# Kernel tuning notes

Measured on AMD Instinct MI355X. Metric: run time of the kernel, lower is better.

The kernel has to match this reference:

```python
import jax, jax.numpy as jnp
import numpy as np

PI = 3.1415926
CHAINS = [[0, 2, 5, 8, 11], [0, 1, 4, 7, 10], [0, 3, 6, 9, 12, 15], [9, 14, 17, 19, 21], [9, 13, 16, 18, 20]]
NUM_JOINTS = 22
CTX = 512
B = 131072


def setup_inputs() -> dict:
    key = jax.random.key(0)
    k_ctx, k_w0, k_b0, k_w, k_b = jax.random.split(key, 5)
    context_vec = jax.random.normal(k_ctx, (B, CTX), dtype=jnp.float32)
    # root linear: context_size -> 3
    W0 = jax.random.normal(k_w0, (CTX, 3), dtype=jnp.float32) * 0.02
    b0 = jax.random.normal(k_b0, (3,), dtype=jnp.float32) * 0.02
    # non-root linears: (context_size + 3) -> 3, stacked per joint index (row 0 unused)
    W = jax.random.normal(k_w, (NUM_JOINTS, CTX + 3, 3), dtype=jnp.float32) * 0.02
    b = jax.random.normal(k_b, (NUM_JOINTS, 3), dtype=jnp.float32) * 0.02
    return {"context_vec": context_vec, "W0": W0, "b0": b0, "W": W, "b": b}


def reference(context_vec, W0, b0, W, b):
    # Sequential per-joint tiny linears along kinematic chains (do_all_parent=False):
    # each child consumes [context, parent_joint(3)] -> 3, then tanh * PI.
    joints = [None] * NUM_JOINTS
    joints[0] = jnp.tanh(context_vec @ W0 + b0) * PI  # [B, 3]
    for chain in CHAINS:
        for j in range(1, len(chain)):
            jid = chain[j]
            inp = jnp.concatenate([context_vec, joints[chain[j - 1]]], axis=-1)  # [B, CTX+3]
            joints[jid] = jnp.tanh(inp @ W[jid] + b[jid]) * PI
    return jnp.concatenate(joints, axis=-1)  # [B, 3*NUM_JOINTS]
```

## Files before the change

### kernel.cpp

```cpp
#include <hip/hip_runtime.h>
#include <cstdint>
#include <cstddef>


#define CTXD 512
#define NCOL 66
#define KT   16
#define NT   5
#define NCH  8
#define RPB  128
#define LDS_STRIDE 67

typedef __attribute__((ext_vector_type(8))) short  short8;
typedef __attribute__((ext_vector_type(4))) float  f32x4;

__device__ __forceinline__ unsigned short f2bf(float x) {
  unsigned u = __float_as_uint(x);
  return (unsigned short)((u + 0x7FFFu + ((u >> 16) & 1u)) >> 16);
}

__device__ __forceinline__ unsigned cvt2(float a, float b) {
  unsigned r;
  asm("v_cvt_pk_bf16_f32 %0, %1, %2" : "=v"(r) : "v"(a), "v"(b));
  return r;
}

__device__ __forceinline__ float tanhpi(float x) {
  float t = exp2f(x * 2.885390081777927f);
  return 3.1415926f - 6.2831852f * __builtin_amdgcn_rcpf(t + 1.0f);
}

__global__ void prep_wfrag(const float* __restrict__ W0,
                           const float* __restrict__ W,
                           unsigned short* __restrict__ wf) {
  int idx = blockIdx.x * blockDim.x + threadIdx.x;
  if (idx >= KT * NT * 64 * 8) return;
  int j    = idx & 7;
  int lane = (idx >> 3) & 63;
  int rest = idx >> 9;
  int nt   = rest % NT;
  int kt   = rest / NT;
  int k    = kt * 32 + (lane >> 4) * 8 + j;
  int col  = nt * 16 + (lane & 15);
  float v = 0.f;
  if (col < 3)          v = W0[k * 3 + col];
  else if (col < NCOL)  v = W[(col / 3) * (515 * 3) + k * 3 + (col % 3)];
  wf[idx] = f2bf(v);
}

__global__ __launch_bounds__(256, 4) void hdl_main(
    const float* __restrict__ ctx,
    const float* __restrict__ b0,
    const float* __restrict__ W,
    const float* __restrict__ bflat,
    const unsigned short* __restrict__ wf,
    float* __restrict__ out)
{
  __shared__ float smem[RPB * LDS_STRIDE];

  const int tid  = threadIdx.x;
  const int lane = tid & 63;
  const int wave = tid >> 6;
  const int r16  = lane & 15;
  const int kg   = lane >> 4;
  const long blockRow = (long)blockIdx.x * RPB;

  f32x4 acc[2][NT] = {};

  float bias[NT];
#pragma unroll
  for (int n = 0; n < NT; ++n) {
    int col = n * 16 + r16;
    bias[n] = (col < 3) ? b0[col] : ((col < NCOL) ? bflat[col] : 0.f);
  }

  float* stage = smem + wave * 2048;
  const float* srcBase =
      ctx + (blockRow + wave * 32 + (lane >> 4)) * (long)CTXD + (lane & 15) * 4;

  for (int c = 0; c < NCH; ++c) {
#pragma unroll
    for (int j = 0; j < 8; ++j) {
      const float* s = srcBase + (size_t)j * 4 * CTXD + c * 64;
      __builtin_amdgcn_global_load_lds(
          (const __attribute__((address_space(1))) void*)s,
          (__attribute__((address_space(3))) void*)(stage + j * 256),
          16, 0, 0);
    }
    asm volatile("s_waitcnt vmcnt(0)" ::: "memory");

#pragma unroll
    for (int t = 0; t < 2; ++t) {
      const int kt = c * 2 + t;
      short8 bfr[NT];
#pragma unroll
      for (int n = 0; n < NT; ++n)
        bfr[n] = *(const short8*)(wf + (size_t)((kt * NT + n) * 64 + lane) * 8);

#pragma unroll
      for (int m = 0; m < 2; ++m) {
        const float* fp = stage + (m * 16 + r16) * 64 + t * 32 + kg * 8;
        float4 f0 = *(const float4*)(fp);
        float4 f1 = *(const float4*)(fp + 4);
        union { short8 s; unsigned u[4]; } A;
        A.u[0] = cvt2(f0.x, f0.y);
        A.u[1] = cvt2(f0.z, f0.w);
        A.u[2] = cvt2(f1.x, f1.y);
        A.u[3] = cvt2(f1.z, f1.w);
#pragma unroll
        for (int n = 0; n < NT; ++n)
          acc[m][n] = __builtin_amdgcn_mfma_f32_16x16x32_bf16(
              A.s, bfr[n], acc[m][n], 0, 0, 0);
      }
    }
    asm volatile("" ::: "memory");
  }

  __syncthreads();

#pragma unroll
  for (int m = 0; m < 2; ++m) {
#pragma unroll
    for (int n = 0; n < NT; ++n) {
      int col = n * 16 + r16;
      if (col < NCOL) {
        int rb = wave * 32 + m * 16 + kg * 4;
#pragma unroll
        for (int q = 0; q < 4; ++q)
          smem[(rb + q) * LDS_STRIDE + col] = acc[m][n][q] + bias[n];
      }
    }
  }
  __syncthreads();

  if (tid < RPB) {
    float* row = smem + tid * LDS_STRIDE;
    float J[22][3];
#pragma unroll
    for (int cc = 0; cc < 3; ++cc) J[0][cc] = tanhpi(row[cc]);

    constexpr int EP[21] = {0,2,5,8, 0,1,4,7, 0,3,6,9,12, 9,14,17,19, 9,13,16,18};
    constexpr int EC[21] = {2,5,8,11, 1,4,7,10, 3,6,9,12,15, 14,17,19,21, 13,16,18,20};
#pragma unroll
    for (int e = 0; e < 21; ++e) {
      const int p  = EP[e];
      const int ch = EC[e];
      const float* wp = W + ch * 1545 + 1536;
#pragma unroll
      for (int cc = 0; cc < 3; ++cc) {
        float s = row[3 * ch + cc];
        s += J[p][0] * wp[cc] + J[p][1] * wp[3 + cc] + J[p][2] * wp[6 + cc];
        J[ch][cc] = tanhpi(s);
      }
    }
#pragma unroll
    for (int jj = 0; jj < 22; ++jj)
#pragma unroll
      for (int cc = 0; cc < 3; ++cc) row[3 * jj + cc] = J[jj][cc];
  }
  __syncthreads();

  const size_t outBase = (size_t)blockRow * NCOL;
  for (int i = tid; i < RPB * NCOL; i += 256) {
    int r = i / NCOL;
    int cc = i - r * NCOL;
    out[outBase + i] = smem[r * LDS_STRIDE + cc];
  }
}

extern "C" void kernel_launch(void* const* d_in, const int* in_sizes, int n_in,
                              void* d_out, int out_size, void* d_ws, size_t ws_size,
                              hipStream_t stream) {
  const float* ctx  = (const float*)d_in[0];
  const float* W0   = (const float*)d_in[1];
  const float* b0   = (const float*)d_in[2];
  const float* W    = (const float*)d_in[3];
  const float* bfl  = (const float*)d_in[4];
  unsigned short* wf = (unsigned short*)d_ws;

  int prep_elems = KT * NT * 64 * 8;
  hipLaunchKernelGGL(prep_wfrag, dim3((prep_elems + 255) / 256), dim3(256), 0,
                     stream, W0, W, wf);

  int nrows = out_size / NCOL;
  hipLaunchKernelGGL(hdl_main, dim3(nrows / RPB), dim3(256), 0,
                     stream, ctx, b0, W, bfl, wf, (float*)d_out);
}
```

Baseline: 64.04 us.

## Double-buffer per-wave LDS staging with XOR-swizzled layout

Result: no change. 63.73 us (-0.5%).

```diff
diff --git a/kernel.cpp b/kernel.cpp
--- a/kernel.cpp
+++ b/kernel.cpp
@@ -7,7 +7,6 @@
 #define NCOL 66
 #define KT   16
 #define NT   5
-#define NCH  8
 #define RPB  128
 #define LDS_STRIDE 67
 
@@ -76,44 +75,57 @@
 
   float* stage = smem + wave * 2048;
   const float* srcBase =
-      ctx + (blockRow + wave * 32 + (lane >> 4)) * (long)CTXD + (lane & 15) * 4;
-
-  for (int c = 0; c < NCH; ++c) {
-#pragma unroll
-    for (int j = 0; j < 8; ++j) {
-      const float* s = srcBase + (size_t)j * 4 * CTXD + c * 64;
-      __builtin_amdgcn_global_load_lds(
-          (const __attribute__((address_space(1))) void*)s,
-          (__attribute__((address_space(3))) void*)(stage + j * 256),
-          16, 0, 0);
-    }
-    asm volatile("s_waitcnt vmcnt(0)" ::: "memory");
-
-#pragma unroll
-    for (int t = 0; t < 2; ++t) {
-      const int kt = c * 2 + t;
-      short8 bfr[NT];
+      ctx + (blockRow + wave * 32 + (lane >> 3)) * (long)CTXD
+          + (((lane & 7) ^ (lane >> 3)) << 2);
+
+#define ISSUE_GLL(ktv, buf)                                                    \
+  {                                                                            \
+    _Pragma("unroll")                                                          \
+    for (int j = 0; j < 4; ++j) {                                              \
+      const float* s = srcBase + (size_t)(j * 8) * CTXD + (ktv) * 32;          \
+      __builtin_amdgcn_global_load_lds(                                        \
+          (const __attribute__((address_space(1))) void*)s,                    \
+          (__attribute__((address_space(3))) void*)((buf) + j * 256),          \
+          16, 0, 0);                                                           \
+    }                                                                          \
+  }
+
+  ISSUE_GLL(0, stage)
+
+#pragma unroll
+  for (int kt = 0; kt < KT; ++kt) {
+    const float* cur = stage + (kt & 1) * 1024;
+    float* nxt = stage + ((kt + 1) & 1) * 1024;
+
+    short8 bfr[NT];
+#pragma unroll
+    for (int n = 0; n < NT; ++n)
+      bfr[n] = *(const short8*)(wf + (size_t)((kt * NT + n) * 64 + lane) * 8);
+
+    if (kt < KT - 1) {
+      ISSUE_GLL(kt + 1, nxt)
+      asm volatile("s_waitcnt vmcnt(4)" ::: "memory");
+    } else {
+      asm volatile("s_waitcnt vmcnt(0)" ::: "memory");
+    }
+
+#pragma unroll
+    for (int m = 0; m < 2; ++m) {
+      const int row = m * 16 + r16;
+      const float* rbase = cur + row * 32;
+      const int rx = r16 & 7;
+      float4 f0 = *(const float4*)(rbase + ((((kg * 2)     ) ^ rx) << 2));
+      float4 f1 = *(const float4*)(rbase + ((((kg * 2) + 1 ) ^ rx) << 2));
+      union { short8 s; unsigned u[4]; } A;
+      A.u[0] = cvt2(f0.x, f0.y);
+      A.u[1] = cvt2(f0.z, f0.w);
+      A.u[2] = cvt2(f1.x, f1.y);
+      A.u[3] = cvt2(f1.z, f1.w);
 #pragma unroll
       for (int n = 0; n < NT; ++n)
-        bfr[n] = *(const short8*)(wf + (size_t)((kt * NT + n) * 64 + lane) * 8);
-
-#pragma unroll
-      for (int m = 0; m < 2; ++m) {
-        const float* fp = stage + (m * 16 + r16) * 64 + t * 32 + kg * 8;
-        float4 f0 = *(const float4*)(fp);
-        float4 f1 = *(const float4*)(fp + 4);
-        union { short8 s; unsigned u[4]; } A;
-        A.u[0] = cvt2(f0.x, f0.y);
-        A.u[1] = cvt2(f0.z, f0.w);
-        A.u[2] = cvt2(f1.x, f1.y);
-        A.u[3] = cvt2(f1.z, f1.w);
-#pragma unroll
-        for (int n = 0; n < NT; ++n)
-          acc[m][n] = __builtin_amdgcn_mfma_f32_16x16x32_bf16(
-              A.s, bfr[n], acc[m][n], 0, 0, 0);
-      }
-    }
-    asm volatile("" ::: "memory");
+        acc[m][n] = __builtin_amdgcn_mfma_f32_16x16x32_bf16(
+            A.s, bfr[n], acc[m][n], 0, 0, 0);
+    }
   }
 
   __syncthreads();
```

## Switch to single-wave blocks of 16 rows with full-row async LDS staging

Applied to the files above, without the earlier changes.

Measured after the change: 112.4 us. 1.76x slower.

```diff
diff --git a/kernel.cpp b/kernel.cpp
--- a/kernel.cpp
+++ b/kernel.cpp
@@ -7,8 +7,7 @@
 #define NCOL 66
 #define KT   16
 #define NT   5
-#define NCH  8
-#define RPB  128
+#define RPB  16
 #define LDS_STRIDE 67
 
 typedef __attribute__((ext_vector_type(8))) short  short8;
@@ -48,7 +47,7 @@
   wf[idx] = f2bf(v);
 }
 
-__global__ __launch_bounds__(256, 4) void hdl_main(
+__global__ __launch_bounds__(64) void hdl_main(
     const float* __restrict__ ctx,
     const float* __restrict__ b0,
     const float* __restrict__ W,
@@ -56,16 +55,68 @@
     const unsigned short* __restrict__ wf,
     float* __restrict__ out)
 {
-  __shared__ float smem[RPB * LDS_STRIDE];
+  __shared__ float smem[RPB * CTXD];
 
-  const int tid  = threadIdx.x;
-  const int lane = tid & 63;
-  const int wave = tid >> 6;
+  const int lane = threadIdx.x;
   const int r16  = lane & 15;
   const int kg   = lane >> 4;
+  const int rx   = r16 & 7;
   const long blockRow = (long)blockIdx.x * RPB;
 
-  f32x4 acc[2][NT] = {};
+  f32x4 acc[NT] = {};
+
+  short8 bfr0[NT];
+#pragma unroll
+  for (int n = 0; n < NT; ++n)
+    bfr0[n] = *(const short8*)(wf + (size_t)(n * 64 + lane) * 8);
+  asm volatile("" ::: "memory");
+
+#pragma unroll
+  for (int h = 0; h < 2; ++h) {
+#pragma unroll
+    for (int r = 0; r < RPB; ++r) {
+      const float* s = ctx + (blockRow + r) * CTXD + h * 256
+                           + ((lane ^ (r & 7)) << 2);
+      __builtin_amdgcn_global_load_lds(
+          (const __attribute__((address_space(1))) void*)s,
+          (__attribute__((address_space(3))) void*)(smem + r * CTXD + h * 256),
+          16, 0, 0);
+    }
+    asm volatile("" ::: "memory");
+  }
+
+  asm volatile("s_waitcnt vmcnt(16)" ::: "memory");
+
+#pragma unroll
+  for (int kt = 0; kt < KT; ++kt) {
+    if (kt == 8)
+      asm volatile("s_waitcnt vmcnt(0)" ::: "memory");
+
+    short8 bfr[NT];
+    if (kt == 0) {
+#pragma unroll
+      for (int n = 0; n < NT; ++n) bfr[n] = bfr0[n];
+    } else {
+#pragma unroll
+      for (int n = 0; n < NT; ++n)
+        bfr[n] = *(const short8*)(wf + (size_t)((kt * NT + n) * 64 + lane) * 8);
+    }
+
+    const int g0 = kt * 8 + kg * 2;
+    const char* rowb = (const char*)smem + r16 * 2048;
+    float4 f0 = *(const float4*)(rowb + (size_t)((g0       ^ rx) << 4));
+    float4 f1 = *(const float4*)(rowb + (size_t)(((g0 + 1) ^ rx) << 4));
+    union { short8 s; unsigned u[4]; } A;
+    A.u[0] = cvt2(f0.x, f0.y);
+    A.u[1] = cvt2(f0.z, f0.w);
+    A.u[2] = cvt2(f1.x, f1.y);
+    A.u[3] = cvt2(f1.z, f1.w);
+#pragma unroll
+    for (int n = 0; n < NT; ++n)
+      acc[n] = __builtin_amdgcn_mfma_f32_16x16x32_bf16(A.s, bfr[n], acc[n],
+                                                       0, 0, 0);
+  }
+  __syncthreads();
 
   float bias[NT];
 #pragma unroll
@@ -74,67 +125,19 @@
     bias[n] = (col < 3) ? b0[col] : ((col < NCOL) ? bflat[col] : 0.f);
   }
 
-  float* stage = smem + wave * 2048;
-  const float* srcBase =
-      ctx + (blockRow + wave * 32 + (lane >> 4)) * (long)CTXD + (lane & 15) * 4;
-
-  for (int c = 0; c < NCH; ++c) {
 #pragma unroll
-    for (int j = 0; j < 8; ++j) {
-      const float* s = srcBase + (size_t)j * 4 * CTXD + c * 64;
-      __builtin_amdgcn_global_load_lds(
-          (const __attribute__((address_space(1))) void*)s,
-          (__attribute__((address_space(3))) void*)(stage + j * 256),
-          16, 0, 0);
-    }
-    asm volatile("s_waitcnt vmcnt(0)" ::: "memory");
-
+  for (int n = 0; n < NT; ++n) {
+    int col = n * 16 + r16;
+    if (col < NCOL) {
 #pragma unroll
-    for (int t = 0; t < 2; ++t) {
-      const int kt = c * 2 + t;
-      short8 bfr[NT];
-#pragma unroll
-      for (int n = 0; n < NT; ++n)
-        bfr[n] = *(const short8*)(wf + (size_t)((kt * NT + n) * 64 + lane) * 8);
-
-#pragma unroll
-      for (int m = 0; m < 2; ++m) {
-        const float* fp = stage + (m * 16 + r16) * 64 + t * 32 + kg * 8;
-        float4 f0 = *(const float4*)(fp);
-        float4 f1 = *(const float4*)(fp + 4);
-        union { short8 s; unsigned u[4]; } A;
-        A.u[0] = cvt2(f0.x, f0.y);
-        A.u[1] = cvt2(f0.z, f0.w);
-        A.u[2] = cvt2(f1.x, f1.y);
-        A.u[3] = cvt2(f1.z, f1.w);
-#pragma unroll
-        for (int n = 0; n < NT; ++n)
-          acc[m][n] = __builtin_amdgcn_mfma_f32_16x16x32_bf16(
-              A.s, bfr[n], acc[m][n], 0, 0, 0);
-      }
-    }
-    asm volatile("" ::: "memory");
-  }
-
-  __syncthreads();
-
-#pragma unroll
-  for (int m = 0; m < 2; ++m) {
-#pragma unroll
-    for (int n = 0; n < NT; ++n) {
-      int col = n * 16 + r16;
-      if (col < NCOL) {
-        int rb = wave * 32 + m * 16 + kg * 4;
-#pragma unroll
-        for (int q = 0; q < 4; ++q)
-          smem[(rb + q) * LDS_STRIDE + col] = acc[m][n][q] + bias[n];
-      }
+      for (int q = 0; q < 4; ++q)
+        smem[(kg * 4 + q) * LDS_STRIDE + col] = acc[n][q] + bias[n];
     }
   }
   __syncthreads();
 
-  if (tid < RPB) {
-    float* row = smem + tid * LDS_STRIDE;
+  if (lane < RPB) {
+    float* row = smem + lane * LDS_STRIDE;
     float J[22][3];
 #pragma unroll
     for (int cc = 0; cc < 3; ++cc) J[0][cc] = tanhpi(row[cc]);
@@ -161,8 +164,8 @@
   __syncthreads();
 
   const size_t outBase = (size_t)blockRow * NCOL;
-  for (int i = tid; i < RPB * NCOL; i += 256) {
-    int r = i / NCOL;
+  for (int i = lane; i < RPB * NCOL; i += 64) {
+    int r  = i / NCOL;
     int cc = i - r * NCOL;
     out[outBase + i] = smem[r * LDS_STRIDE + cc];
   }
@@ -183,6 +186,6 @@
                      stream, W0, W, wf);
 
   int nrows = out_size / NCOL;
-  hipLaunchKernelGGL(hdl_main, dim3(nrows / RPB), dim3(256), 0,
+  hipLaunchKernelGGL(hdl_main, dim3(nrows / RPB), dim3(64), 0,
                      stream, ctx, b0, W, bfl, wf, (float*)d_out);
 }
```
